# Kernel optimization log

Measured on AMD Instinct MI355X. Metric: run time of the kernel, lower is better.

## Reference

```python
import jax, jax.numpy as jnp
import numpy as np

B, S, HID = 8, 2048, 1024
H, DH = 16, 64
EPS = 1e-12  # torch F.normalize eps


def _heads(x):
    # [B,S,HID] -> [B,H,S,DH]
    return x.reshape(B, S, H, DH).transpose(0, 2, 1, 3)


def _l2norm(x):
    n = jnp.sqrt(jnp.sum(x * x, axis=-1, keepdims=True))
    return x / jnp.maximum(n, EPS)


def setup_inputs() -> dict:
    key = jax.random.key(0)
    ks = jax.random.split(key, 4)
    sc = 0.02
    return {
        "hidden_states": jax.random.normal(ks[0], (B, S, HID), jnp.float32),
        "attention_mask": jnp.zeros((B, 1, 1, S), jnp.int32),
        "Wq": jax.random.normal(ks[1], (HID, HID), jnp.float32) * sc,
        "bq": jnp.zeros((HID,), jnp.float32),
        "Wk": jax.random.normal(ks[2], (HID, HID), jnp.float32) * sc,
        "bk": jnp.zeros((HID,), jnp.float32),
        "Wv": jax.random.normal(ks[3], (HID, HID), jnp.float32) * sc,
        "bv": jnp.zeros((HID,), jnp.float32),
    }


def reference(hidden_states, attention_mask, Wq, bq, Wk, bk, Wv, bv):
    # QKV projections (nn.Linear: x @ W^T + b; here W stored as [in,out]-equivalent square)
    q = _heads(hidden_states @ Wq + bq)  # [B,H,S,DH]
    k = _heads(hidden_states @ Wk + bk)
    v = _heads(hidden_states @ Wv + bv)

    # mask == 0 -> valid token; transpose(-1,-2): [B,1,1,S] -> [B,1,S,1]
    mask = (attention_mask == 0).astype(q.dtype)            # [B,1,1,S]
    mask_t = jnp.swapaxes(mask, -1, -2)                      # [B,1,S,1]
    q = q * mask_t
    k = k * mask_t
    v = v * mask_t

    q = _l2norm(q)
    k = _l2norm(k)
    v = v / mask.sum(-1)[..., None]                          # divide by valid-token count

    if q.shape[-1] > q.shape[-2]:
        # DH > S: explicit O(S^2) path
        ctx = jnp.einsum("bhsq,bhqd->bhsd", jnp.einsum("bhse,bhqe->bhsq", q, k), v)
    else:
        # linear-attention order: Q @ (K^T V), O(S*DH^2)
        kv = jnp.einsum("bhse,bhsd->bhed", k, v)             # [B,H,DH,DH]
        ctx = jnp.einsum("bhse,bhed->bhsd", q, kv)

    return ctx.transpose(0, 2, 1, 3).reshape(B, S, HID)
```

## Files before the change

kernel.cpp:

```cpp
#include <hip/hip_runtime.h>
#include <stdint.h>

#define B_    8
#define S_    2048
#define HID_  1024
#define H_    16
#define DH_   64
#define M_    (B_ * S_)

using bf16x8 = __attribute__((ext_vector_type(8))) __bf16;
using bf16x4 = __attribute__((ext_vector_type(4))) __bf16;
using f32x4  = __attribute__((ext_vector_type(4))) float;

__device__ __forceinline__ void gload_lds16(const void* g, void* l) {
  __builtin_amdgcn_global_load_lds(
      (const __attribute__((address_space(1))) void*)g,
      (__attribute__((address_space(3))) void*)l, 16, 0, 0);
}

__global__ __launch_bounds__(256) void prep(
    const float* __restrict__ hs, __bf16* __restrict__ hsb,
    const float* __restrict__ Wq, const float* __restrict__ Wk,
    const float* __restrict__ Wv, __bf16* __restrict__ Wt,
    const int* __restrict__ mask, float* __restrict__ validf,
    float* __restrict__ counts) {
  int bid = blockIdx.x;
  int tid = threadIdx.x;
  if (bid < 2048) {
    int n8 = (B_ * S_ * HID_) / 8;
    int i = bid * 256 + tid;
    int stride = 2048 * 256;
    for (; i < n8; i += stride) {
      const float4* p = (const float4*)(hs + (size_t)i * 8);
      float4 a = p[0], c = p[1];
      bf16x8 v;
      v[0] = (__bf16)a.x; v[1] = (__bf16)a.y; v[2] = (__bf16)a.z; v[3] = (__bf16)a.w;
      v[4] = (__bf16)c.x; v[5] = (__bf16)c.y; v[6] = (__bf16)c.z; v[7] = (__bf16)c.w;
      *(bf16x8*)(hsb + (size_t)i * 8) = v;
    }
  } else if (bid < 5120) {
    __shared__ float tile[32][33];
    int idx = bid - 2048;
    int w = idx >> 10, r = idx & 1023;
    int k0 = (r & 31) * 32, n0 = (r >> 5) * 32;
    const float* W = (w == 0) ? Wq : (w == 1) ? Wk : Wv;
    int tx = tid & 31, ty = tid >> 5;
#pragma unroll
    for (int i = 0; i < 4; ++i)
      tile[ty * 4 + i][tx] = W[(size_t)(k0 + ty * 4 + i) * HID_ + n0 + tx];
    __syncthreads();
#pragma unroll
    for (int i = 0; i < 4; ++i)
      Wt[(size_t)w * HID_ * HID_ + (size_t)(n0 + ty * 4 + i) * HID_ + k0 + tx] =
          (__bf16)tile[tx][ty * 4 + i];
  } else {
    __shared__ float red[256];
    int b = bid - 5120;
    float cnt = 0.f;
    for (int s = tid; s < S_; s += 256) {
      float v = (mask[b * S_ + s] == 0) ? 1.f : 0.f;
      validf[b * S_ + s] = v;
      cnt += v;
    }
    red[tid] = cnt;
    __syncthreads();
    for (int off = 128; off > 0; off >>= 1) {
      if (tid < off) red[tid] += red[tid + off];
      __syncthreads();
    }
    if (tid == 0) counts[b] = red[0];
  }
}

__global__ __launch_bounds__(512, 2) void qkv_gemm8(
    const __bf16* __restrict__ hsb, const __bf16* __restrict__ Wt,
    const float* __restrict__ biasq, const float* __restrict__ biask,
    const float* __restrict__ biasv, const float* __restrict__ validf,
    const float* __restrict__ counts, __bf16* __restrict__ qn,
    __bf16* __restrict__ kT, __bf16* __restrict__ vT) {
  __shared__ __bf16 As[2][2][128 * 64];
  __shared__ __bf16 Bs[2][2][128 * 64];

  int bid = blockIdx.x;
  int swz = (bid & 7) * 96 + (bid >> 3);
  int tm = swz / 12;
  int tnw = swz - tm * 12;
  int tn = tnw & 3;
  int w  = tnw >> 2;

  int tid = threadIdx.x;
  int lane = tid & 63, wid = tid >> 6;
  int lr = lane & 15, g = lane >> 4;
  int wr = wid >> 2, wcn = wid & 3;

  int m0 = tm * 256, n0 = tn * 256;
  const __bf16* Bsrc = Wt + (size_t)w * (HID_ * HID_);

  int srow = tid >> 3;
  int scol = ((tid & 7) ^ (srow & 7)) << 3;
  int soff = tid * 16;

  auto stA = [&](int t_, int ah) {
    const __bf16* s0 = hsb + (size_t)(m0 + ah * 128 + srow) * HID_ + t_ * 64 + scol;
    char* d = (char*)&As[t_ & 1][ah][0] + soff;
    gload_lds16(s0, d);
    gload_lds16(s0 + (size_t)64 * HID_, d + 8192);
  };
  auto stB = [&](int t_, int bh) {
    const __bf16* s0 = Bsrc + (size_t)(n0 + bh * 128 + srow) * HID_ + t_ * 64 + scol;
    char* d = (char*)&Bs[t_ & 1][bh][0] + soff;
    gload_lds16(s0, d);
    gload_lds16(s0 + (size_t)64 * HID_, d + 8192);
  };

  int swz8 = (lr & 7) << 4;
  int arow = wr * 64 + lr;
  int brow = (wcn & 1) * 64 + lr;
  int bsel = wcn >> 1;

  f32x4 acc[8][4] = {};
  bf16x8 fb[4], fbN[4], fa0[4], fa1[4];

#define RD_A(DST, BUF, MH, KK)                                                \
  _Pragma("unroll")                                                           \
  for (int mf = 0; mf < 4; ++mf)                                              \
    DST[mf] = *(const bf16x8*)((const char*)&As[BUF][MH][0] +                 \
                               (arow + mf * 16) * 128 +                       \
                               (((KK) * 64 + g * 16) ^ swz8));                \
  __builtin_amdgcn_sched_barrier(0);

#define RD_B(DST, BUF, KK)                                                    \
  _Pragma("unroll")                                                           \
  for (int nf = 0; nf < 4; ++nf)                                              \
    DST[nf] = *(const bf16x8*)((const char*)&Bs[BUF][bsel][0] +               \
                               (brow + nf * 16) * 128 +                       \
                               (((KK) * 64 + g * 16) ^ swz8));                \
  __builtin_amdgcn_sched_barrier(0);

#define CLUSTER(ACCB, FA, FB, LG)                                             \
  asm volatile("s_waitcnt lgkmcnt(" #LG ")" ::: "memory");                    \
  __builtin_amdgcn_sched_barrier(0);                                          \
  __builtin_amdgcn_s_setprio(1);                                              \
  _Pragma("unroll")                                                           \
  for (int mf = 0; mf < 4; ++mf)                                              \
    _Pragma("unroll")                                                         \
    for (int nf = 0; nf < 4; ++nf)                                            \
      acc[(ACCB) + mf][nf] = __builtin_amdgcn_mfma_f32_16x16x32_bf16(         \
          FA[mf], FB[nf], acc[(ACCB) + mf][nf], 0, 0, 0);                     \
  __builtin_amdgcn_s_setprio(0);                                              \
  __builtin_amdgcn_sched_barrier(0);

  stA(0, 0); stA(0, 1); stB(0, 0); stB(0, 1);

#pragma unroll 2
  for (int t = 0; t < 16; ++t) {
    int buf = t & 1;
    asm volatile("s_waitcnt vmcnt(0)" ::: "memory");
    __builtin_amdgcn_s_barrier();
    __builtin_amdgcn_sched_barrier(0);

    RD_B(fb,  buf, 0);
    RD_A(fa0, buf, 0, 0);
    RD_A(fa1, buf, 1, 0);
    if (t < 15) { stA(t + 1, 0); stA(t + 1, 1); }

    CLUSTER(0, fa0, fb, 4)

    RD_B(fbN, buf, 1);
    RD_A(fa0, buf, 0, 1);
    if (t < 15) stB(t + 1, 0);

    CLUSTER(4, fa1, fb, 8)

    RD_A(fa1, buf, 1, 1);
    if (t < 15) stB(t + 1, 1);

    CLUSTER(0, fa0, fbN, 4)
    CLUSTER(4, fa1, fbN, 0)
  }
#undef RD_A
#undef RD_B
#undef CLUSTER

  const float* bias = (w == 0) ? biasq : (w == 1) ? biask : biasv;
  float bb[4];
#pragma unroll
  for (int nf = 0; nf < 4; ++nf) bb[nf] = bias[n0 + wcn * 64 + nf * 16 + lr];

  int batch = m0 >> 11;
  float invcnt = 1.0f / counts[batch];
  int h = tn * 4 + wcn;

#pragma unroll
  for (int m = 0; m < 8; ++m) {
    int mh = m >> 2, mf = m & 3;
    int rbase = m0 + mh * 128 + wr * 64 + mf * 16 + g * 4;
    float vld[4];
#pragma unroll
    for (int j = 0; j < 4; ++j) vld[j] = validf[rbase + j];
    float ss[4] = {0.f, 0.f, 0.f, 0.f};
#pragma unroll
    for (int nf = 0; nf < 4; ++nf)
#pragma unroll
      for (int j = 0; j < 4; ++j) {
        float x = (acc[m][nf][j] + bb[nf]) * vld[j];
        acc[m][nf][j] = x;
        ss[j] += x * x;
      }
    float sc[4];
#pragma unroll
    for (int j = 0; j < 4; ++j) {
      float s = ss[j];
      s += __shfl_xor(s, 1);
      s += __shfl_xor(s, 2);
      s += __shfl_xor(s, 4);
      s += __shfl_xor(s, 8);
      if (w == 2) sc[j] = vld[j] * invcnt;
      else        sc[j] = 1.0f / fmaxf(sqrtf(s), 1e-12f);
    }
    if (w == 0) {
#pragma unroll
      for (int nf = 0; nf < 4; ++nf) {
        int c = n0 + wcn * 64 + nf * 16 + lr;
#pragma unroll
        for (int j = 0; j < 4; ++j)
          qn[(size_t)(rbase + j) * HID_ + c] = (__bf16)(acc[m][nf][j] * sc[j]);
      }
    } else {
      __bf16* dst = (w == 1) ? kT : vT;
      int sbase = rbase & (S_ - 1);
#pragma unroll
      for (int nf = 0; nf < 4; ++nf) {
        int d = nf * 16 + lr;
        bf16x4 pk;
#pragma unroll
        for (int j = 0; j < 4; ++j) pk[j] = (__bf16)(acc[m][nf][j] * sc[j]);
        *(bf16x4*)(dst + (size_t)((batch * H_ + h) * DH_ + d) * S_ + sbase) = pk;
      }
    }
  }
}

__global__ __launch_bounds__(256) void kv_gemm(const __bf16* __restrict__ kT,
                                               const __bf16* __restrict__ vT,
                                               float* __restrict__ vkp) {
  __shared__ __align__(16) char smem[65536];
  __bf16* kbuf = (__bf16*)smem;
  __bf16* vbuf = (__bf16*)(smem + 32768);

  int bh = blockIdx.x & 127, half = blockIdx.x >> 7;
  int tid = threadIdx.x, lane = tid & 63, wid = tid >> 6;
  int g = lane >> 4, lr = lane & 15;
  const __bf16* kb = kT + (size_t)bh * DH_ * S_;
  const __bf16* vb = vT + (size_t)bh * DH_ * S_;

  f32x4 acc[4][4] = {};

  int sbeg = half * (S_ / 2);
  for (int sc0 = sbeg; sc0 < sbeg + S_ / 2; sc0 += 256) {
#pragma unroll
    for (int it = 0; it < 8; ++it) {
      int seg = tid + it * 256;
      int row = seg >> 5, col = (seg & 31) * 8;
      gload_lds16(kb + (size_t)row * S_ + sc0 + col, (void*)(kbuf + seg * 8));
      gload_lds16(vb + (size_t)row * S_ + sc0 + col, (void*)(vbuf + seg * 8));
    }
    __syncthreads();
    int sl = wid * 64;
#pragma unroll
    for (int kk = 0; kk < 64; kk += 32) {
      bf16x8 fa[4], fb[4];
#pragma unroll
      for (int m = 0; m < 4; ++m)
        fa[m] = *(const bf16x8*)(vbuf + (m * 16 + lr) * 256 + sl + kk + g * 8);
#pragma unroll
      for (int n = 0; n < 4; ++n)
        fb[n] = *(const bf16x8*)(kbuf + (n * 16 + lr) * 256 + sl + kk + g * 8);
#pragma unroll
      for (int m = 0; m < 4; ++m)
#pragma unroll
        for (int n = 0; n < 4; ++n)
          acc[m][n] = __builtin_amdgcn_mfma_f32_16x16x32_bf16(fa[m], fb[n], acc[m][n], 0, 0, 0);
    }
    __syncthreads();
  }

  float* red = (float*)smem;
#pragma unroll
  for (int m = 0; m < 4; ++m)
#pragma unroll
    for (int n = 0; n < 4; ++n)
#pragma unroll
      for (int j = 0; j < 4; ++j)
        red[wid * 4096 + (m * 16 + g * 4 + j) * 64 + n * 16 + lr] = acc[m][n][j];
  __syncthreads();
  for (int idx = tid; idx < 4096; idx += 256) {
    float s = red[idx] + red[4096 + idx] + red[8192 + idx] + red[12288 + idx];
    vkp[(size_t)(half * 128 + bh) * 4096 + idx] = s;
  }
}

__global__ __launch_bounds__(256) void ctx_gemm(const __bf16* __restrict__ qn,
                                                const float* __restrict__ vkp,
                                                float* __restrict__ out) {
  __shared__ __align__(16) __bf16 qbuf[128 * 64];
  __shared__ __align__(16) __bf16 wbuf[64 * 64];

  int st = blockIdx.x;
  int bh = blockIdx.y;
  int b = bh >> 4, h = bh & 15;
  int tid = threadIdx.x, lane = tid & 63, wid = tid >> 6;
  int g = lane >> 4, lr = lane & 15;
  int s0 = st * 128;

#pragma unroll
  for (int it = 0; it < 4; ++it) {
    int seg = tid + it * 256;
    int row = seg >> 3, col = (seg & 7) * 8;
    gload_lds16(qn + (size_t)(b * S_ + s0 + row) * HID_ + h * DH_ + col,
                (void*)(qbuf + seg * 8));
  }
  {
    const float* p0 = vkp + (size_t)bh * 4096;
    const float* p1 = p0 + 524288;
#pragma unroll
    for (int it = 0; it < 2; ++it) {
      int i = tid * 8 + it * 2048;
      f32x4 a0 = *(const f32x4*)(p0 + i);
      f32x4 a1 = *(const f32x4*)(p0 + i + 4);
      f32x4 c0 = *(const f32x4*)(p1 + i);
      f32x4 c1 = *(const f32x4*)(p1 + i + 4);
      bf16x8 v;
#pragma unroll
      for (int j = 0; j < 4; ++j) {
        v[j]     = (__bf16)(a0[j] + c0[j]);
        v[4 + j] = (__bf16)(a1[j] + c1[j]);
      }
      *(bf16x8*)(wbuf + i) = v;
    }
  }
  __syncthreads();

  f32x4 acc[2][4] = {};
#pragma unroll
  for (int kk = 0; kk < 64; kk += 32) {
    bf16x8 fa[2], fb[4];
#pragma unroll
    for (int m = 0; m < 2; ++m)
      fa[m] = *(const bf16x8*)(qbuf + (wid * 32 + m * 16 + lr) * 64 + kk + g * 8);
#pragma unroll
    for (int n = 0; n < 4; ++n)
      fb[n] = *(const bf16x8*)(wbuf + (n * 16 + lr) * 64 + kk + g * 8);
#pragma unroll
    for (int m = 0; m < 2; ++m)
#pragma unroll
      for (int n = 0; n < 4; ++n)
        acc[m][n] = __builtin_amdgcn_mfma_f32_16x16x32_bf16(fa[m], fb[n], acc[m][n], 0, 0, 0);
  }

#pragma unroll
  for (int m = 0; m < 2; ++m) {
    int rbase = s0 + wid * 32 + m * 16 + g * 4;
#pragma unroll
    for (int n = 0; n < 4; ++n) {
      int d = n * 16 + lr;
#pragma unroll
      for (int j = 0; j < 4; ++j)
        out[(size_t)(b * S_ + rbase + j) * HID_ + h * DH_ + d] = acc[m][n][j];
    }
  }
}

extern "C" void kernel_launch(void* const* d_in, const int* in_sizes, int n_in,
                              void* d_out, int out_size, void* d_ws, size_t ws_size,
                              hipStream_t stream) {
  const float* hs   = (const float*)d_in[0];
  const int*   mask = (const int*)d_in[1];
  const float* Wq   = (const float*)d_in[2];
  const float* bq   = (const float*)d_in[3];
  const float* Wk   = (const float*)d_in[4];
  const float* bk   = (const float*)d_in[5];
  const float* Wv   = (const float*)d_in[6];
  const float* bv   = (const float*)d_in[7];
  float* out = (float*)d_out;

  char* ws = (char*)d_ws;
  __bf16* hsb    = (__bf16*)(ws);
  __bf16* Wt     = (__bf16*)(ws + (33554432));
  __bf16* qn     = (__bf16*)(ws + (41943040));
  __bf16* kT     = (__bf16*)(ws + (75497472));
  __bf16* vT     = (__bf16*)(ws + (109051904));
  float*  validf = (float*)(ws + (143654912));
  float*  counts = (float*)(ws + (143654912) + 65536);
  float*  vkp    = (float*)(ws + (33554432));

  prep<<<5128, 256, 0, stream>>>(hs, hsb, Wq, Wk, Wv, Wt, mask, validf, counts);
  qkv_gemm8<<<768, 512, 0, stream>>>(hsb, Wt, bq, bk, bv, validf, counts, qn, kT, vT);
  kv_gemm<<<256, 256, 0, stream>>>(kT, vT, vkp);
  ctx_gemm<<<dim3(16, 128), 256, 0, stream>>>(qn, vkp, out);
}
```

Before: 176.8 us.

## Use 4-wave QKV GEMM with 128x128 per-wave tiles instead of 8 waves

Rewrites the QKV projection GEMM to use 256 threads (4 waves) per 256x256 block, each wave computing a 128x128 sub-tile with 8x8 MFMA accumulators instead of 64x64 pieces across 8 waves. Loads are spread over four issues per thread and the LDS-read/MFMA interleave is rescheduled. This raises per-wave arithmetic intensity and cuts LDS fragment reads per MFMA. The cost is a much larger register footprint (256 accumulator floats) and lower occupancy, which may hurt latency hiding.

```diff
diff --git a/kernel.cpp b/kernel.cpp
--- a/kernel.cpp
+++ b/kernel.cpp
@@ -72,7 +72,7 @@
   }
 }
 
-__global__ __launch_bounds__(512, 2) void qkv_gemm8(
+__global__ __launch_bounds__(256, 1) void qkv_gemm4(
     const __bf16* __restrict__ hsb, const __bf16* __restrict__ Wt,
     const float* __restrict__ biasq, const float* __restrict__ biask,
     const float* __restrict__ biasv, const float* __restrict__ validf,
@@ -91,62 +91,63 @@
   int tid = threadIdx.x;
   int lane = tid & 63, wid = tid >> 6;
   int lr = lane & 15, g = lane >> 4;
-  int wr = wid >> 2, wcn = wid & 3;
+  int wr = wid >> 1, wcn = wid & 1;
 
   int m0 = tm * 256, n0 = tn * 256;
   const __bf16* Bsrc = Wt + (size_t)w * (HID_ * HID_);
 
-  int srow = tid >> 3;
-  int scol = ((tid & 7) ^ (srow & 7)) << 3;
-  int soff = tid * 16;
-
   auto stA = [&](int t_, int ah) {
-    const __bf16* s0 = hsb + (size_t)(m0 + ah * 128 + srow) * HID_ + t_ * 64 + scol;
-    char* d = (char*)&As[t_ & 1][ah][0] + soff;
-    gload_lds16(s0, d);
-    gload_lds16(s0 + (size_t)64 * HID_, d + 8192);
+#pragma unroll
+    for (int j = 0; j < 4; ++j) {
+      int seg = tid + j * 256;
+      int row = seg >> 3;
+      int col = ((seg & 7) ^ (row & 7)) << 3;
+      gload_lds16(hsb + (size_t)(m0 + ah * 128 + row) * HID_ + t_ * 64 + col,
+                  (char*)&As[t_ & 1][ah][0] + seg * 16);
+    }
   };
   auto stB = [&](int t_, int bh) {
-    const __bf16* s0 = Bsrc + (size_t)(n0 + bh * 128 + srow) * HID_ + t_ * 64 + scol;
-    char* d = (char*)&Bs[t_ & 1][bh][0] + soff;
-    gload_lds16(s0, d);
-    gload_lds16(s0 + (size_t)64 * HID_, d + 8192);
+#pragma unroll
+    for (int j = 0; j < 4; ++j) {
+      int seg = tid + j * 256;
+      int row = seg >> 3;
+      int col = ((seg & 7) ^ (row & 7)) << 3;
+      gload_lds16(Bsrc + (size_t)(n0 + bh * 128 + row) * HID_ + t_ * 64 + col,
+                  (char*)&Bs[t_ & 1][bh][0] + seg * 16);
+    }
   };
 
   int swz8 = (lr & 7) << 4;
-  int arow = wr * 64 + lr;
-  int brow = (wcn & 1) * 64 + lr;
-  int bsel = wcn >> 1;
-
-  f32x4 acc[8][4] = {};
-  bf16x8 fb[4], fbN[4], fa0[4], fa1[4];
-
-#define RD_A(DST, BUF, MH, KK)                                                \
+
+  f32x4 acc[8][8] = {};
+  bf16x8 fa[8], fb[8], fbN[8];
+
+#define RD_A8(DST, BUF, KK)                                                   \
   _Pragma("unroll")                                                           \
-  for (int mf = 0; mf < 4; ++mf)                                              \
-    DST[mf] = *(const bf16x8*)((const char*)&As[BUF][MH][0] +                 \
-                               (arow + mf * 16) * 128 +                       \
+  for (int mf = 0; mf < 8; ++mf)                                              \
+    DST[mf] = *(const bf16x8*)((const char*)&As[BUF][wr][0] +                 \
+                               (mf * 16 + lr) * 128 +                         \
                                (((KK) * 64 + g * 16) ^ swz8));                \
   __builtin_amdgcn_sched_barrier(0);
 
-#define RD_B(DST, BUF, KK)                                                    \
+#define RD_B8(DST, BUF, KK)                                                   \
   _Pragma("unroll")                                                           \
-  for (int nf = 0; nf < 4; ++nf)                                              \
-    DST[nf] = *(const bf16x8*)((const char*)&Bs[BUF][bsel][0] +               \
-                               (brow + nf * 16) * 128 +                       \
+  for (int nf = 0; nf < 8; ++nf)                                              \
+    DST[nf] = *(const bf16x8*)((const char*)&Bs[BUF][wcn][0] +                \
+                               (nf * 16 + lr) * 128 +                         \
                                (((KK) * 64 + g * 16) ^ swz8));                \
   __builtin_amdgcn_sched_barrier(0);
 
-#define CLUSTER(ACCB, FA, FB, LG)                                             \
+#define CLUSTER(MF0, FA, FB, LG)                                              \
   asm volatile("s_waitcnt lgkmcnt(" #LG ")" ::: "memory");                    \
   __builtin_amdgcn_sched_barrier(0);                                          \
   __builtin_amdgcn_s_setprio(1);                                              \
   _Pragma("unroll")                                                           \
-  for (int mf = 0; mf < 4; ++mf)                                              \
+  for (int mi = 0; mi < 4; ++mi)                                              \
     _Pragma("unroll")                                                         \
-    for (int nf = 0; nf < 4; ++nf)                                            \
-      acc[(ACCB) + mf][nf] = __builtin_amdgcn_mfma_f32_16x16x32_bf16(         \
-          FA[mf], FB[nf], acc[(ACCB) + mf][nf], 0, 0, 0);                     \
+    for (int nf = 0; nf < 8; ++nf)                                            \
+      acc[(MF0) + mi][nf] = __builtin_amdgcn_mfma_f32_16x16x32_bf16(          \
+          FA[(MF0) + mi], FB[nf], acc[(MF0) + mi][nf], 0, 0, 0);              \
   __builtin_amdgcn_s_setprio(0);                                              \
   __builtin_amdgcn_sched_barrier(0);
 
@@ -159,82 +160,81 @@
     __builtin_amdgcn_s_barrier();
     __builtin_amdgcn_sched_barrier(0);
 
-    RD_B(fb,  buf, 0);
-    RD_A(fa0, buf, 0, 0);
-    RD_A(fa1, buf, 1, 0);
-    if (t < 15) { stA(t + 1, 0); stA(t + 1, 1); }
-
-    CLUSTER(0, fa0, fb, 4)
-
-    RD_B(fbN, buf, 1);
-    RD_A(fa0, buf, 0, 1);
+    RD_B8(fb, buf, 0);
+    RD_A8(fa, buf, 0);
+    if (t < 15) stA(t + 1, 0);
+
+    CLUSTER(0, fa, fb, 4)
+    if (t < 15) stA(t + 1, 1);
+    RD_B8(fbN, buf, 1);
+
+    CLUSTER(4, fa, fb, 8)
+    RD_A8(fa, buf, 1);
     if (t < 15) stB(t + 1, 0);
 
-    CLUSTER(4, fa1, fb, 8)
-
-    RD_A(fa1, buf, 1, 1);
+    CLUSTER(0, fa, fbN, 4)
     if (t < 15) stB(t + 1, 1);
-
-    CLUSTER(0, fa0, fbN, 4)
-    CLUSTER(4, fa1, fbN, 0)
-  }
-#undef RD_A
-#undef RD_B
+    CLUSTER(4, fa, fbN, 0)
+  }
+#undef RD_A8
+#undef RD_B8
 #undef CLUSTER
 
   const float* bias = (w == 0) ? biasq : (w == 1) ? biask : biasv;
-  float bb[4];
-#pragma unroll
-  for (int nf = 0; nf < 4; ++nf) bb[nf] = bias[n0 + wcn * 64 + nf * 16 + lr];
+  float bb[8];
+#pragma unroll
+  for (int nf = 0; nf < 8; ++nf) bb[nf] = bias[n0 + wcn * 128 + nf * 16 + lr];
 
   int batch = m0 >> 11;
   float invcnt = 1.0f / counts[batch];
-  int h = tn * 4 + wcn;
-
-#pragma unroll
-  for (int m = 0; m < 8; ++m) {
-    int mh = m >> 2, mf = m & 3;
-    int rbase = m0 + mh * 128 + wr * 64 + mf * 16 + g * 4;
+  int hbase = tn * 4 + wcn * 2;
+
+#pragma unroll
+  for (int mf = 0; mf < 8; ++mf) {
+    int rbase = m0 + wr * 128 + mf * 16 + g * 4;
     float vld[4];
 #pragma unroll
     for (int j = 0; j < 4; ++j) vld[j] = validf[rbase + j];
-    float ss[4] = {0.f, 0.f, 0.f, 0.f};
-#pragma unroll
-    for (int nf = 0; nf < 4; ++nf)
+    float ss[2][4] = {};
+#pragma unroll
+    for (int nf = 0; nf < 8; ++nf)
 #pragma unroll
       for (int j = 0; j < 4; ++j) {
-        float x = (acc[m][nf][j] + bb[nf]) * vld[j];
-        acc[m][nf][j] = x;
-        ss[j] += x * x;
+        float x = (acc[mf][nf][j] + bb[nf]) * vld[j];
+        acc[mf][nf][j] = x;
+        ss[nf >> 2][j] += x * x;
       }
-    float sc[4];
-#pragma unroll
-    for (int j = 0; j < 4; ++j) {
-      float s = ss[j];
-      s += __shfl_xor(s, 1);
-      s += __shfl_xor(s, 2);
-      s += __shfl_xor(s, 4);
-      s += __shfl_xor(s, 8);
-      if (w == 2) sc[j] = vld[j] * invcnt;
-      else        sc[j] = 1.0f / fmaxf(sqrtf(s), 1e-12f);
-    }
+    float sc[2][4];
+#pragma unroll
+    for (int hh = 0; hh < 2; ++hh)
+#pragma unroll
+      for (int j = 0; j < 4; ++j) {
+        float s = ss[hh][j];
+        s += __shfl_xor(s, 1);
+        s += __shfl_xor(s, 2);
+        s += __shfl_xor(s, 4);
+        s += __shfl_xor(s, 8);
+        if (w == 2) sc[hh][j] = vld[j] * invcnt;
+        else        sc[hh][j] = 1.0f / fmaxf(sqrtf(s), 1e-12f);
+      }
     if (w == 0) {
 #pragma unroll
-      for (int nf = 0; nf < 4; ++nf) {
-        int c = n0 + wcn * 64 + nf * 16 + lr;
+      for (int nf = 0; nf < 8; ++nf) {
+        int c = n0 + wcn * 128 + nf * 16 + lr;
 #pragma unroll
         for (int j = 0; j < 4; ++j)
-          qn[(size_t)(rbase + j) * HID_ + c] = (__bf16)(acc[m][nf][j] * sc[j]);
+          qn[(size_t)(rbase + j) * HID_ + c] = (__bf16)(acc[mf][nf][j] * sc[nf >> 2][j]);
       }
     } else {
       __bf16* dst = (w == 1) ? kT : vT;
       int sbase = rbase & (S_ - 1);
 #pragma unroll
-      for (int nf = 0; nf < 4; ++nf) {
-        int d = nf * 16 + lr;
+      for (int nf = 0; nf < 8; ++nf) {
+        int d = (nf & 3) * 16 + lr;
+        int h = hbase + (nf >> 2);
         bf16x4 pk;
 #pragma unroll
-        for (int j = 0; j < 4; ++j) pk[j] = (__bf16)(acc[m][nf][j] * sc[j]);
+        for (int j = 0; j < 4; ++j) pk[j] = (__bf16)(acc[mf][nf][j] * sc[nf >> 2][j]);
         *(bf16x4*)(dst + (size_t)((batch * H_ + h) * DH_ + d) * S_ + sbase) = pk;
       }
     }
@@ -395,7 +395,7 @@
   float*  vkp    = (float*)(ws + (33554432));
 
   prep<<<5128, 256, 0, stream>>>(hs, hsb, Wq, Wk, Wv, Wt, mask, validf, counts);
-  qkv_gemm8<<<768, 512, 0, stream>>>(hsb, Wt, bq, bk, bv, validf, counts, qn, kT, vT);
+  qkv_gemm4<<<768, 256, 0, stream>>>(hsb, Wt, bq, bk, bv, validf, counts, qn, kT, vT);
   kv_gemm<<<256, 256, 0, stream>>>(kT, vT, vkp);
   ctx_gemm<<<dim3(16, 128), 256, 0, stream>>>(qn, vkp, out);
 }
```

Measured after the change: 398.9 us. 126% more time.

## Restructure QKV GEMM main loop into barrier-staged 8-wave ping-pong pipeline

Applied to the files above, without the earlier changes.

Rewrites the projection GEMM K-loop so LDS fragment reads for the next phase and the next tile are prefetched ahead of each MFMA cluster. Global-to-LDS loads are issued earlier with partial vmcnt waits, and s_barriers are placed around every MFMA cluster so waves alternate between memory and compute phases. The goal is to hide LDS and global latency behind matrix work. In exchange it adds many more workgroup barriers, and the hand-tuned wait counts are fragile: the buffer being overwritten must already be consumed before the loads that target it.

```diff
diff --git a/kernel.cpp b/kernel.cpp
--- a/kernel.cpp
+++ b/kernel.cpp
@@ -119,9 +119,9 @@
   int bsel = wcn >> 1;
 
   f32x4 acc[8][4] = {};
-  bf16x8 fb[4], fbN[4], fa0[4], fa1[4];
-
-#define RD_A(DST, BUF, MH, KK)                                                \
+  bf16x8 faX[4], faY[4], fb0[4], fb1[4];
+
+#define RD_FA(DST, BUF, MH, KK)                                               \
   _Pragma("unroll")                                                           \
   for (int mf = 0; mf < 4; ++mf)                                              \
     DST[mf] = *(const bf16x8*)((const char*)&As[BUF][MH][0] +                 \
@@ -129,7 +129,7 @@
                                (((KK) * 64 + g * 16) ^ swz8));                \
   __builtin_amdgcn_sched_barrier(0);
 
-#define RD_B(DST, BUF, KK)                                                    \
+#define RD_FB(DST, BUF, KK)                                                   \
   _Pragma("unroll")                                                           \
   for (int nf = 0; nf < 4; ++nf)                                              \
     DST[nf] = *(const bf16x8*)((const char*)&Bs[BUF][bsel][0] +               \
@@ -150,36 +150,50 @@
   __builtin_amdgcn_s_setprio(0);                                              \
   __builtin_amdgcn_sched_barrier(0);
 
-  stA(0, 0); stA(0, 1); stB(0, 0); stB(0, 1);
-
-#pragma unroll 2
+  stB(0, 0); stB(0, 1); stA(0, 0); stA(0, 1);
+  asm volatile("s_waitcnt vmcnt(2)" ::: "memory");
+  __builtin_amdgcn_s_barrier();
+  __builtin_amdgcn_sched_barrier(0);
+  RD_FA(faX, 0, 0, 0)
+  RD_FB(fb0, 0, 0)
+
   for (int t = 0; t < 16; ++t) {
-    int buf = t & 1;
-    asm volatile("s_waitcnt vmcnt(0)" ::: "memory");
-    __builtin_amdgcn_s_barrier();
+    int buf = t & 1, nbuf = buf ^ 1;
+
+    if (t < 15) {
+      stB(t + 1, 0); stB(t + 1, 1); stA(t + 1, 0);
+      asm volatile("s_waitcnt vmcnt(6)" ::: "memory");
+    } else {
+      asm volatile("s_waitcnt vmcnt(0)" ::: "memory");
+    }
     __builtin_amdgcn_sched_barrier(0);
-
-    RD_B(fb,  buf, 0);
-    RD_A(fa0, buf, 0, 0);
-    RD_A(fa1, buf, 1, 0);
-    if (t < 15) { stA(t + 1, 0); stA(t + 1, 1); }
-
-    CLUSTER(0, fa0, fb, 4)
-
-    RD_B(fbN, buf, 1);
-    RD_A(fa0, buf, 0, 1);
-    if (t < 15) stB(t + 1, 0);
-
-    CLUSTER(4, fa1, fb, 8)
-
-    RD_A(fa1, buf, 1, 1);
-    if (t < 15) stB(t + 1, 1);
-
-    CLUSTER(0, fa0, fbN, 4)
-    CLUSTER(4, fa1, fbN, 0)
-  }
-#undef RD_A
-#undef RD_B
+    RD_FA(faY, buf, 0, 1)
+    RD_FB(fb1, buf, 1)
+    __builtin_amdgcn_s_barrier();
+    CLUSTER(0, faX, fb0, 8)
+    __builtin_amdgcn_s_barrier();
+
+    if (t < 15) stA(t + 1, 1);
+    RD_FA(faX, buf, 1, 0)
+    __builtin_amdgcn_s_barrier();
+    CLUSTER(0, faY, fb1, 4)
+    __builtin_amdgcn_s_barrier();
+
+    asm volatile("s_waitcnt vmcnt(2)" ::: "memory");
+    __builtin_amdgcn_sched_barrier(0);
+    RD_FA(faY, buf, 1, 1)
+    __builtin_amdgcn_s_barrier();
+    CLUSTER(4, faX, fb0, 4)
+    __builtin_amdgcn_s_barrier();
+
+    RD_FA(faX, nbuf, 0, 0)
+    RD_FB(fb0, nbuf, 0)
+    __builtin_amdgcn_s_barrier();
+    CLUSTER(4, faY, fb1, 8)
+    __builtin_amdgcn_s_barrier();
+  }
+#undef RD_FA
+#undef RD_FB
 #undef CLUSTER
 
   const float* bias = (w == 0) ? biasq : (w == 1) ? biask : biasv;
```

Result: slower. 199.2 us (+12.7%).
